# Performance work log

Hardware: AMD Instinct MI355X
Metric: run time of the kernel (lower is better)

Reference implementation:

```python
import jax, jax.numpy as jnp
import numpy as np

PAD = (2, 2)  # from kernel=[1,3,3,1], sampling_factor_padding=2, kernel_size=3


def _make_kernel(k1d):
    k = np.asarray(k1d, dtype=np.float32)
    k2d = k[None, :] * k[:, None]
    return jnp.asarray(k2d / k2d.sum())


def setup_inputs() -> dict:
    key = jax.random.key(0)
    x = jax.random.normal(key, (8, 256, 256, 256), dtype=jnp.float32)
    kernel = _make_kernel([1, 3, 3, 1])  # [4,4] normalized FIR kernel (buffer)
    return {"x": x, "kernel": kernel}


def reference(x, kernel):
    # upfirdn2d with up=1, down=1, pad=(2,2): pad then depthwise TRUE convolution
    # (StyleGAN2 flips the kernel before F.conv2d, i.e. real convolution).
    B, C, H, W = x.shape
    kh, kw = kernel.shape
    w = jnp.flip(kernel, (0, 1)).astype(x.dtype)[None, None]  # [1,1,kh,kw]
    w = jnp.broadcast_to(w, (C, 1, kh, kw))  # depthwise: same kernel per channel
    out = jax.lax.conv_general_dilated(
        x, w,
        window_strides=(1, 1),
        padding=(PAD, PAD),
        dimension_numbers=("NCHW", "OIHW", "NCHW"),
        feature_group_count=C,
    )  # [B, C, H+1, W+1] since H + 4 - 4 + 1 = H + 1
    return out
```

## Files before the change

kernel.cpp:

```cpp
#include <hip/hip_runtime.h>


#define IW 256
#define IH 256
#define OW 257
#define OH 257

typedef float f4u __attribute__((vector_size(16), aligned(4)));

__device__ __forceinline__ float sbc(float v) {
    return __uint_as_float(__builtin_amdgcn_readfirstlane(__float_as_uint(v)));
}

__global__ __launch_bounds__(256) void blur_fir_kernel(
    const float* __restrict__ x,
    const float* __restrict__ k2d,
    float* __restrict__ out)
{
    const int tid   = threadIdx.x;
    const int cg    = tid & 63;
    const int strip = tid >> 6;
    const int plane = blockIdx.x;

    const float w0 = sbc(k2d[0]);
    const float w1 = sbc(k2d[1]);
    const float w2 = sbc(k2d[2]);
    const float w3 = sbc(k2d[3]);
    const float inv = 1.0f / w0;
    const float v1 = sbc(k2d[4]  * inv);
    const float v2 = sbc(k2d[8]  * inv);
    const float v3 = sbc(k2d[12] * inv);

    const int   c0 = cg << 2;
    const float mL = (cg > 0)  ? 1.0f : 0.0f;
    const float mR = (cg < 63) ? 1.0f : 0.0f;
    const int   lm = (cg > 0)  ? cg - 1 : 0;
    const int   lp = (cg < 63) ? cg + 1 : 63;

    const float* xp = x + ((size_t)plane << 16);
    const int r0 = strip << 6;

    auto loadraw = [&](int r) -> float4 {
        int rr = min(max(r, 0), IH - 1);
        return *(const float4*)(xp + (rr << 8) + c0);
    };
    auto hcomb = [&](float4 Bv, int r, float4& h, float& h4) {
        float rm = (r >= 0 && r < IH) ? 1.0f : 0.0f;
        float lx = __shfl(Bv.z, lm, 64) * mL;
        float ly = __shfl(Bv.w, lm, 64) * mL;
        float rv = __shfl(Bv.x, lp, 64) * mR;
        h.x = w0 * Bv.y + w1 * Bv.x + w2 * ly   + w3 * lx;
        h.y = w0 * Bv.z + w1 * Bv.y + w2 * Bv.x + w3 * ly;
        h.z = w0 * Bv.w + w1 * Bv.z + w2 * Bv.y + w3 * Bv.x;
        h.w = w0 * rv   + w1 * Bv.w + w2 * Bv.z + w3 * Bv.y;
        h4  = w2 * Bv.w + w3 * Bv.z;
        h.x *= rm; h.y *= rm; h.z *= rm; h.w *= rm; h4 *= rm;
    };
    auto vcomb = [&](float4 a, float4 b, float4 c, float4 d) -> float4 {
        float4 r;
        r.x = a.x + v1 * b.x + v2 * c.x + v3 * d.x;
        r.y = a.y + v1 * b.y + v2 * c.y + v3 * d.y;
        r.z = a.z + v1 * b.z + v2 * c.z + v3 * d.z;
        r.w = a.w + v1 * b.w + v2 * c.w + v3 * d.w;
        return r;
    };

    float4 C0, C1, C2; float sc0, sc1, sc2;
    { float4 B = loadraw(r0 - 2); hcomb(B, r0 - 2, C0, sc0); }
    { float4 B = loadraw(r0 - 1); hcomb(B, r0 - 1, C1, sc1); }
    { float4 B = loadraw(r0    ); hcomb(B, r0    , C2, sc2); }

    float4 G0 = loadraw(r0 + 1);
    float4 G1 = loadraw(r0 + 2);
    float4 G2 = loadraw(r0 + 3);
    float4 G3 = loadraw(r0 + 4);

    float* op = out + (size_t)plane * (OW * OH) + (size_t)r0 * OW + c0;
    const bool last = (cg == 63);

    #pragma unroll 2
    for (int g = 0; g < 16; ++g) {
        const int rb = r0 + (g << 2);
        float4 N0 = loadraw(rb + 5);
        float4 N1 = loadraw(rb + 6);
        float4 N2 = loadraw(rb + 7);
        float4 N3 = loadraw(rb + 8);

        float4 F0, F1, F2, F3; float sf0, sf1, sf2, sf3;
        hcomb(G0, rb + 1, F0, sf0);
        hcomb(G1, rb + 2, F1, sf1);
        hcomb(G2, rb + 3, F2, sf2);
        hcomb(G3, rb + 4, F3, sf3);

        float4 R0 = vcomb(F0, C2, C1, C0);
        float4 R1 = vcomb(F1, F0, C2, C1);
        float4 R2 = vcomb(F2, F1, F0, C2);
        float4 R3 = vcomb(F3, F2, F1, F0);
        *(f4u*)(op         ) = (f4u){R0.x, R0.y, R0.z, R0.w};
        *(f4u*)(op +     OW) = (f4u){R1.x, R1.y, R1.z, R1.w};
        *(f4u*)(op + 2 * OW) = (f4u){R2.x, R2.y, R2.z, R2.w};
        *(f4u*)(op + 3 * OW) = (f4u){R3.x, R3.y, R3.z, R3.w};
        if (last) {
            op[4]          = sf0 + v1 * sc2 + v2 * sc1 + v3 * sc0;
            op[OW + 4]     = sf1 + v1 * sf0 + v2 * sc2 + v3 * sc1;
            op[2 * OW + 4] = sf2 + v1 * sf1 + v2 * sf0 + v3 * sc2;
            op[3 * OW + 4] = sf3 + v1 * sf2 + v2 * sf1 + v3 * sf0;
        }
        op += 4 * OW;

        C0 = F1;  C1 = F2;  C2 = F3;
        sc0 = sf1; sc1 = sf2; sc2 = sf3;
        G0 = N0; G1 = N1; G2 = N2; G3 = N3;
    }

    if (strip == 3) {
        float4 R;
        R.x = v1 * C2.x + v2 * C1.x + v3 * C0.x;
        R.y = v1 * C2.y + v2 * C1.y + v3 * C0.y;
        R.z = v1 * C2.z + v2 * C1.z + v3 * C0.z;
        R.w = v1 * C2.w + v2 * C1.w + v3 * C0.w;
        *(f4u*)op = (f4u){R.x, R.y, R.z, R.w};
        if (last) op[4] = v1 * sc2 + v2 * sc1 + v3 * sc0;
    }
}

extern "C" void kernel_launch(void* const* d_in, const int* in_sizes, int n_in,
                              void* d_out, int out_size, void* d_ws, size_t ws_size,
                              hipStream_t stream) {
    const float* x   = (const float*)d_in[0];
    const float* k2d = (const float*)d_in[1];
    float* out = (float*)d_out;

    int nplanes = in_sizes[0] >> 16;
    blur_fir_kernel<<<nplanes, 256, 0, stream>>>(x, k2d, out);
}
```

Baseline: 247.4 us.

## Process two planes per block with deeper 8-row register pipeline

Each block now handles two consecutive planes in sequence and half as many blocks are launched. The inner row loop advances 8 rows per iteration with 8 prefetched rows in flight instead of 4, and launch bounds request 4 waves per SIMD. The goal is more outstanding loads per wave to hide memory latency and less per-block setup cost. In exchange it uses more registers, risks a tighter occupancy limit, and halves the block count, which reduces parallelism across CUs (1024 blocks).

```diff
diff --git a/kernel.cpp b/kernel.cpp
--- a/kernel.cpp
+++ b/kernel.cpp
@@ -12,7 +12,7 @@
     return __uint_as_float(__builtin_amdgcn_readfirstlane(__float_as_uint(v)));
 }
 
-__global__ __launch_bounds__(256) void blur_fir_kernel(
+__global__ __launch_bounds__(256, 4) void blur_fir_kernel(
     const float* __restrict__ x,
     const float* __restrict__ k2d,
     float* __restrict__ out)
@@ -20,7 +20,6 @@
     const int tid   = threadIdx.x;
     const int cg    = tid & 63;
     const int strip = tid >> 6;
-    const int plane = blockIdx.x;
 
     const float w0 = sbc(k2d[0]);
     const float w1 = sbc(k2d[1]);
@@ -36,91 +35,111 @@
     const float mR = (cg < 63) ? 1.0f : 0.0f;
     const int   lm = (cg > 0)  ? cg - 1 : 0;
     const int   lp = (cg < 63) ? cg + 1 : 63;
-
-    const float* xp = x + ((size_t)plane << 16);
-    const int r0 = strip << 6;
-
-    auto loadraw = [&](int r) -> float4 {
-        int rr = min(max(r, 0), IH - 1);
-        return *(const float4*)(xp + (rr << 8) + c0);
-    };
-    auto hcomb = [&](float4 Bv, int r, float4& h, float& h4) {
-        float rm = (r >= 0 && r < IH) ? 1.0f : 0.0f;
-        float lx = __shfl(Bv.z, lm, 64) * mL;
-        float ly = __shfl(Bv.w, lm, 64) * mL;
-        float rv = __shfl(Bv.x, lp, 64) * mR;
-        h.x = w0 * Bv.y + w1 * Bv.x + w2 * ly   + w3 * lx;
-        h.y = w0 * Bv.z + w1 * Bv.y + w2 * Bv.x + w3 * ly;
-        h.z = w0 * Bv.w + w1 * Bv.z + w2 * Bv.y + w3 * Bv.x;
-        h.w = w0 * rv   + w1 * Bv.w + w2 * Bv.z + w3 * Bv.y;
-        h4  = w2 * Bv.w + w3 * Bv.z;
-        h.x *= rm; h.y *= rm; h.z *= rm; h.w *= rm; h4 *= rm;
-    };
-    auto vcomb = [&](float4 a, float4 b, float4 c, float4 d) -> float4 {
-        float4 r;
-        r.x = a.x + v1 * b.x + v2 * c.x + v3 * d.x;
-        r.y = a.y + v1 * b.y + v2 * c.y + v3 * d.y;
-        r.z = a.z + v1 * b.z + v2 * c.z + v3 * d.z;
-        r.w = a.w + v1 * b.w + v2 * c.w + v3 * d.w;
-        return r;
-    };
-
-    float4 C0, C1, C2; float sc0, sc1, sc2;
-    { float4 B = loadraw(r0 - 2); hcomb(B, r0 - 2, C0, sc0); }
-    { float4 B = loadraw(r0 - 1); hcomb(B, r0 - 1, C1, sc1); }
-    { float4 B = loadraw(r0    ); hcomb(B, r0    , C2, sc2); }
-
-    float4 G0 = loadraw(r0 + 1);
-    float4 G1 = loadraw(r0 + 2);
-    float4 G2 = loadraw(r0 + 3);
-    float4 G3 = loadraw(r0 + 4);
-
-    float* op = out + (size_t)plane * (OW * OH) + (size_t)r0 * OW + c0;
+    const int   r0 = strip << 6;
     const bool last = (cg == 63);
 
-    #pragma unroll 2
-    for (int g = 0; g < 16; ++g) {
-        const int rb = r0 + (g << 2);
-        float4 N0 = loadraw(rb + 5);
-        float4 N1 = loadraw(rb + 6);
-        float4 N2 = loadraw(rb + 7);
-        float4 N3 = loadraw(rb + 8);
+    for (int pp = 0; pp < 2; ++pp) {
+        const int plane = (blockIdx.x << 1) + pp;
+        const float* xp = x + ((size_t)plane << 16);
 
-        float4 F0, F1, F2, F3; float sf0, sf1, sf2, sf3;
-        hcomb(G0, rb + 1, F0, sf0);
-        hcomb(G1, rb + 2, F1, sf1);
-        hcomb(G2, rb + 3, F2, sf2);
-        hcomb(G3, rb + 4, F3, sf3);
+        auto loadraw = [&](int r) -> float4 {
+            int rr = min(max(r, 0), IH - 1);
+            return *(const float4*)(xp + (rr << 8) + c0);
+        };
+        auto hcomb = [&](float4 Bv, int r, float4& h, float& h4) {
+            float rm = (r >= 0 && r < IH) ? 1.0f : 0.0f;
+            float lx = __shfl(Bv.z, lm, 64) * mL;
+            float ly = __shfl(Bv.w, lm, 64) * mL;
+            float rv = __shfl(Bv.x, lp, 64) * mR;
+            h.x = w0 * Bv.y + w1 * Bv.x + w2 * ly   + w3 * lx;
+            h.y = w0 * Bv.z + w1 * Bv.y + w2 * Bv.x + w3 * ly;
+            h.z = w0 * Bv.w + w1 * Bv.z + w2 * Bv.y + w3 * Bv.x;
+            h.w = w0 * rv   + w1 * Bv.w + w2 * Bv.z + w3 * Bv.y;
+            h4  = w2 * Bv.w + w3 * Bv.z;
+            h.x *= rm; h.y *= rm; h.z *= rm; h.w *= rm; h4 *= rm;
+        };
+        auto vcomb = [&](float4 a, float4 b, float4 c, float4 d) -> float4 {
+            float4 r;
+            r.x = a.x + v1 * b.x + v2 * c.x + v3 * d.x;
+            r.y = a.y + v1 * b.y + v2 * c.y + v3 * d.y;
+            r.z = a.z + v1 * b.z + v2 * c.z + v3 * d.z;
+            r.w = a.w + v1 * b.w + v2 * c.w + v3 * d.w;
+            return r;
+        };
 
-        float4 R0 = vcomb(F0, C2, C1, C0);
-        float4 R1 = vcomb(F1, F0, C2, C1);
-        float4 R2 = vcomb(F2, F1, F0, C2);
-        float4 R3 = vcomb(F3, F2, F1, F0);
-        *(f4u*)(op         ) = (f4u){R0.x, R0.y, R0.z, R0.w};
-        *(f4u*)(op +     OW) = (f4u){R1.x, R1.y, R1.z, R1.w};
-        *(f4u*)(op + 2 * OW) = (f4u){R2.x, R2.y, R2.z, R2.w};
-        *(f4u*)(op + 3 * OW) = (f4u){R3.x, R3.y, R3.z, R3.w};
-        if (last) {
-            op[4]          = sf0 + v1 * sc2 + v2 * sc1 + v3 * sc0;
-            op[OW + 4]     = sf1 + v1 * sf0 + v2 * sc2 + v3 * sc1;
-            op[2 * OW + 4] = sf2 + v1 * sf1 + v2 * sf0 + v3 * sc2;
-            op[3 * OW + 4] = sf3 + v1 * sf2 + v2 * sf1 + v3 * sf0;
+        float4 C0, C1, C2; float sc0, sc1, sc2;
+        { float4 B = loadraw(r0 - 2); hcomb(B, r0 - 2, C0, sc0); }
+        { float4 B = loadraw(r0 - 1); hcomb(B, r0 - 1, C1, sc1); }
+        { float4 B = loadraw(r0    ); hcomb(B, r0    , C2, sc2); }
+        float4 G0 = loadraw(r0 + 1), G1 = loadraw(r0 + 2);
+        float4 G2 = loadraw(r0 + 3), G3 = loadraw(r0 + 4);
+        float4 G4 = loadraw(r0 + 5), G5 = loadraw(r0 + 6);
+        float4 G6 = loadraw(r0 + 7), G7 = loadraw(r0 + 8);
+
+        float* op = out + (size_t)plane * (OW * OH) + (size_t)r0 * OW + c0;
+
+        #pragma unroll 2
+        for (int g = 0; g < 8; ++g) {
+            const int rb = r0 + (g << 3);
+            float4 N0 = loadraw(rb + 9),  N1 = loadraw(rb + 10);
+            float4 N2 = loadraw(rb + 11), N3 = loadraw(rb + 12);
+            float4 N4 = loadraw(rb + 13), N5 = loadraw(rb + 14);
+            float4 N6 = loadraw(rb + 15), N7 = loadraw(rb + 16);
+
+            float4 F0, F1, F2, F3, F4, F5, F6, F7;
+            float  sf0, sf1, sf2, sf3, sf4, sf5, sf6, sf7;
+            hcomb(G0, rb + 1, F0, sf0);
+            hcomb(G1, rb + 2, F1, sf1);
+            hcomb(G2, rb + 3, F2, sf2);
+            hcomb(G3, rb + 4, F3, sf3);
+            hcomb(G4, rb + 5, F4, sf4);
+            hcomb(G5, rb + 6, F5, sf5);
+            hcomb(G6, rb + 7, F6, sf6);
+            hcomb(G7, rb + 8, F7, sf7);
+
+            float4 R0 = vcomb(F0, C2, C1, C0);
+            float4 R1 = vcomb(F1, F0, C2, C1);
+            float4 R2 = vcomb(F2, F1, F0, C2);
+            float4 R3 = vcomb(F3, F2, F1, F0);
+            float4 R4 = vcomb(F4, F3, F2, F1);
+            float4 R5 = vcomb(F5, F4, F3, F2);
+            float4 R6 = vcomb(F6, F5, F4, F3);
+            float4 R7 = vcomb(F7, F6, F5, F4);
+            *(f4u*)(op         ) = (f4u){R0.x, R0.y, R0.z, R0.w};
+            *(f4u*)(op +     OW) = (f4u){R1.x, R1.y, R1.z, R1.w};
+            *(f4u*)(op + 2 * OW) = (f4u){R2.x, R2.y, R2.z, R2.w};
+            *(f4u*)(op + 3 * OW) = (f4u){R3.x, R3.y, R3.z, R3.w};
+            *(f4u*)(op + 4 * OW) = (f4u){R4.x, R4.y, R4.z, R4.w};
+            *(f4u*)(op + 5 * OW) = (f4u){R5.x, R5.y, R5.z, R5.w};
+            *(f4u*)(op + 6 * OW) = (f4u){R6.x, R6.y, R6.z, R6.w};
+            *(f4u*)(op + 7 * OW) = (f4u){R7.x, R7.y, R7.z, R7.w};
+            if (last) {
+                op[4]          = sf0 + v1 * sc2 + v2 * sc1 + v3 * sc0;
+                op[OW + 4]     = sf1 + v1 * sf0 + v2 * sc2 + v3 * sc1;
+                op[2 * OW + 4] = sf2 + v1 * sf1 + v2 * sf0 + v3 * sc2;
+                op[3 * OW + 4] = sf3 + v1 * sf2 + v2 * sf1 + v3 * sf0;
+                op[4 * OW + 4] = sf4 + v1 * sf3 + v2 * sf2 + v3 * sf1;
+                op[5 * OW + 4] = sf5 + v1 * sf4 + v2 * sf3 + v3 * sf2;
+                op[6 * OW + 4] = sf6 + v1 * sf5 + v2 * sf4 + v3 * sf3;
+                op[7 * OW + 4] = sf7 + v1 * sf6 + v2 * sf5 + v3 * sf4;
+            }
+            op += 8 * OW;
+
+            C0 = F5;  C1 = F6;  C2 = F7;
+            sc0 = sf5; sc1 = sf6; sc2 = sf7;
+            G0 = N0; G1 = N1; G2 = N2; G3 = N3;
+            G4 = N4; G5 = N5; G6 = N6; G7 = N7;
         }
-        op += 4 * OW;
 
-        C0 = F1;  C1 = F2;  C2 = F3;
-        sc0 = sf1; sc1 = sf2; sc2 = sf3;
-        G0 = N0; G1 = N1; G2 = N2; G3 = N3;
-    }
-
-    if (strip == 3) {
-        float4 R;
-        R.x = v1 * C2.x + v2 * C1.x + v3 * C0.x;
-        R.y = v1 * C2.y + v2 * C1.y + v3 * C0.y;
-        R.z = v1 * C2.z + v2 * C1.z + v3 * C0.z;
-        R.w = v1 * C2.w + v2 * C1.w + v3 * C0.w;
-        *(f4u*)op = (f4u){R.x, R.y, R.z, R.w};
-        if (last) op[4] = v1 * sc2 + v2 * sc1 + v3 * sc0;
+        if (strip == 3) {
+            float4 R;
+            R.x = v1 * C2.x + v2 * C1.x + v3 * C0.x;
+            R.y = v1 * C2.y + v2 * C1.y + v3 * C0.y;
+            R.z = v1 * C2.z + v2 * C1.z + v3 * C0.z;
+            R.w = v1 * C2.w + v2 * C1.w + v3 * C0.w;
+            *(f4u*)op = (f4u){R.x, R.y, R.z, R.w};
+            if (last) op[4] = v1 * sc2 + v2 * sc1 + v3 * sc0;
+        }
     }
 }
 
@@ -132,5 +151,6 @@
     float* out = (float*)d_out;
 
     int nplanes = in_sizes[0] >> 16;
-    blur_fir_kernel<<<nplanes, 256, 0, stream>>>(x, k2d, out);
+    int nblocks = nplanes >> 1;
+    blur_fir_kernel<<<nblocks, 256, 0, stream>>>(x, k2d, out);
 }
```

Result: slower. 272.2 us (+10.0%).

## Split work into 4-row wave tasks with grid-stride persistent scheduling

Applied to the files above, without the earlier changes.

Replaces the one-block-per-plane layout, where each wave streams 64 rows, with a grid of 2048 blocks whose waves take independent tasks of 4 output rows each in a grid-stride loop. Each task reloads its 7 input rows, so no horizontal results are carried between tasks. This aims to even out load balance and memory-level parallelism across CUs. In exchange, about 7/4 times as many input rows are read and horizontally filtered, which relies on L2 to absorb the overlapping reads.

```diff
diff --git a/kernel.cpp b/kernel.cpp
--- a/kernel.cpp
+++ b/kernel.cpp
@@ -5,6 +5,7 @@
 #define IH 256
 #define OW 257
 #define OH 257
+#define NG 65
 
 typedef float f4u __attribute__((vector_size(16), aligned(4)));
 
@@ -15,12 +16,11 @@
 __global__ __launch_bounds__(256) void blur_fir_kernel(
     const float* __restrict__ x,
     const float* __restrict__ k2d,
-    float* __restrict__ out)
+    float* __restrict__ out,
+    int ntasks, int nwaves)
 {
-    const int tid   = threadIdx.x;
-    const int cg    = tid & 63;
-    const int strip = tid >> 6;
-    const int plane = blockIdx.x;
+    const int lane = threadIdx.x & 63;
+    const int gw   = (blockIdx.x << 2) + (threadIdx.x >> 6);
 
     const float w0 = sbc(k2d[0]);
     const float w1 = sbc(k2d[1]);
@@ -31,96 +31,87 @@
     const float v2 = sbc(k2d[8]  * inv);
     const float v3 = sbc(k2d[12] * inv);
 
-    const int   c0 = cg << 2;
-    const float mL = (cg > 0)  ? 1.0f : 0.0f;
-    const float mR = (cg < 63) ? 1.0f : 0.0f;
-    const int   lm = (cg > 0)  ? cg - 1 : 0;
-    const int   lp = (cg < 63) ? cg + 1 : 63;
+    const int   c0 = lane << 2;
+    const float mL = (lane > 0)  ? 1.0f : 0.0f;
+    const float mR = (lane < 63) ? 1.0f : 0.0f;
+    const int   lm = (lane > 0)  ? lane - 1 : 0;
+    const int   lp = (lane < 63) ? lane + 1 : 63;
+    const bool last = (lane == 63);
 
-    const float* xp = x + ((size_t)plane << 16);
-    const int r0 = strip << 6;
+    for (int t = gw; t < ntasks; t += nwaves) {
+        const int plane = t / NG;
+        const int rg    = t - plane * NG;
+        const float* xp = x + ((size_t)plane << 16);
+        float* op = out + (size_t)plane * (OW * OH) + (size_t)(rg << 2) * OW + c0;
 
-    auto loadraw = [&](int r) -> float4 {
-        int rr = min(max(r, 0), IH - 1);
-        return *(const float4*)(xp + (rr << 8) + c0);
-    };
-    auto hcomb = [&](float4 Bv, int r, float4& h, float& h4) {
-        float rm = (r >= 0 && r < IH) ? 1.0f : 0.0f;
-        float lx = __shfl(Bv.z, lm, 64) * mL;
-        float ly = __shfl(Bv.w, lm, 64) * mL;
-        float rv = __shfl(Bv.x, lp, 64) * mR;
-        h.x = w0 * Bv.y + w1 * Bv.x + w2 * ly   + w3 * lx;
-        h.y = w0 * Bv.z + w1 * Bv.y + w2 * Bv.x + w3 * ly;
-        h.z = w0 * Bv.w + w1 * Bv.z + w2 * Bv.y + w3 * Bv.x;
-        h.w = w0 * rv   + w1 * Bv.w + w2 * Bv.z + w3 * Bv.y;
-        h4  = w2 * Bv.w + w3 * Bv.z;
-        h.x *= rm; h.y *= rm; h.z *= rm; h.w *= rm; h4 *= rm;
-    };
-    auto vcomb = [&](float4 a, float4 b, float4 c, float4 d) -> float4 {
-        float4 r;
-        r.x = a.x + v1 * b.x + v2 * c.x + v3 * d.x;
-        r.y = a.y + v1 * b.y + v2 * c.y + v3 * d.y;
-        r.z = a.z + v1 * b.z + v2 * c.z + v3 * d.z;
-        r.w = a.w + v1 * b.w + v2 * c.w + v3 * d.w;
-        return r;
-    };
+        auto loadraw = [&](int r) -> float4 {
+            int rr = min(max(r, 0), IH - 1);
+            return *(const float4*)(xp + (rr << 8) + c0);
+        };
+        auto hcomb = [&](float4 Bv, int r, float4& h, float& h4) {
+            float rm = (r >= 0 && r < IH) ? 1.0f : 0.0f;
+            float lx = __shfl(Bv.z, lm, 64) * mL;
+            float ly = __shfl(Bv.w, lm, 64) * mL;
+            float rv = __shfl(Bv.x, lp, 64) * mR;
+            h.x = w0 * Bv.y + w1 * Bv.x + w2 * ly   + w3 * lx;
+            h.y = w0 * Bv.z + w1 * Bv.y + w2 * Bv.x + w3 * ly;
+            h.z = w0 * Bv.w + w1 * Bv.z + w2 * Bv.y + w3 * Bv.x;
+            h.w = w0 * rv   + w1 * Bv.w + w2 * Bv.z + w3 * Bv.y;
+            h4  = w2 * Bv.w + w3 * Bv.z;
+            h.x *= rm; h.y *= rm; h.z *= rm; h.w *= rm; h4 *= rm;
+        };
+        auto vcomb = [&](float4 a, float4 b, float4 c, float4 d) -> float4 {
+            float4 r;
+            r.x = a.x + v1 * b.x + v2 * c.x + v3 * d.x;
+            r.y = a.y + v1 * b.y + v2 * c.y + v3 * d.y;
+            r.z = a.z + v1 * b.z + v2 * c.z + v3 * d.z;
+            r.w = a.w + v1 * b.w + v2 * c.w + v3 * d.w;
+            return r;
+        };
 
-    float4 C0, C1, C2; float sc0, sc1, sc2;
-    { float4 B = loadraw(r0 - 2); hcomb(B, r0 - 2, C0, sc0); }
-    { float4 B = loadraw(r0 - 1); hcomb(B, r0 - 1, C1, sc1); }
-    { float4 B = loadraw(r0    ); hcomb(B, r0    , C2, sc2); }
+        if (rg < 64) {
+            const int rb = rg << 2;
+            float4 G0 = loadraw(rb - 2), G1 = loadraw(rb - 1), G2 = loadraw(rb);
+            float4 G3 = loadraw(rb + 1), G4 = loadraw(rb + 2), G5 = loadraw(rb + 3);
+            float4 G6 = loadraw(rb + 4);
 
-    float4 G0 = loadraw(r0 + 1);
-    float4 G1 = loadraw(r0 + 2);
-    float4 G2 = loadraw(r0 + 3);
-    float4 G3 = loadraw(r0 + 4);
+            float4 F0, F1, F2, F3, F4, F5, F6;
+            float  s0, s1, s2, s3, s4, s5, s6;
+            hcomb(G0, rb - 2, F0, s0);
+            hcomb(G1, rb - 1, F1, s1);
+            hcomb(G2, rb    , F2, s2);
+            hcomb(G3, rb + 1, F3, s3);
+            hcomb(G4, rb + 2, F4, s4);
+            hcomb(G5, rb + 3, F5, s5);
+            hcomb(G6, rb + 4, F6, s6);
 
-    float* op = out + (size_t)plane * (OW * OH) + (size_t)r0 * OW + c0;
-    const bool last = (cg == 63);
-
-    #pragma unroll 2
-    for (int g = 0; g < 16; ++g) {
-        const int rb = r0 + (g << 2);
-        float4 N0 = loadraw(rb + 5);
-        float4 N1 = loadraw(rb + 6);
-        float4 N2 = loadraw(rb + 7);
-        float4 N3 = loadraw(rb + 8);
-
-        float4 F0, F1, F2, F3; float sf0, sf1, sf2, sf3;
-        hcomb(G0, rb + 1, F0, sf0);
-        hcomb(G1, rb + 2, F1, sf1);
-        hcomb(G2, rb + 3, F2, sf2);
-        hcomb(G3, rb + 4, F3, sf3);
-
-        float4 R0 = vcomb(F0, C2, C1, C0);
-        float4 R1 = vcomb(F1, F0, C2, C1);
-        float4 R2 = vcomb(F2, F1, F0, C2);
-        float4 R3 = vcomb(F3, F2, F1, F0);
-        *(f4u*)(op         ) = (f4u){R0.x, R0.y, R0.z, R0.w};
-        *(f4u*)(op +     OW) = (f4u){R1.x, R1.y, R1.z, R1.w};
-        *(f4u*)(op + 2 * OW) = (f4u){R2.x, R2.y, R2.z, R2.w};
-        *(f4u*)(op + 3 * OW) = (f4u){R3.x, R3.y, R3.z, R3.w};
-        if (last) {
-            op[4]          = sf0 + v1 * sc2 + v2 * sc1 + v3 * sc0;
-            op[OW + 4]     = sf1 + v1 * sf0 + v2 * sc2 + v3 * sc1;
-            op[2 * OW + 4] = sf2 + v1 * sf1 + v2 * sf0 + v3 * sc2;
-            op[3 * OW + 4] = sf3 + v1 * sf2 + v2 * sf1 + v3 * sf0;
+            float4 R0 = vcomb(F3, F2, F1, F0);
+            float4 R1 = vcomb(F4, F3, F2, F1);
+            float4 R2 = vcomb(F5, F4, F3, F2);
+            float4 R3 = vcomb(F6, F5, F4, F3);
+            *(f4u*)(op         ) = (f4u){R0.x, R0.y, R0.z, R0.w};
+            *(f4u*)(op +     OW) = (f4u){R1.x, R1.y, R1.z, R1.w};
+            *(f4u*)(op + 2 * OW) = (f4u){R2.x, R2.y, R2.z, R2.w};
+            *(f4u*)(op + 3 * OW) = (f4u){R3.x, R3.y, R3.z, R3.w};
+            if (last) {
+                op[4]          = s3 + v1 * s2 + v2 * s1 + v3 * s0;
+                op[OW + 4]     = s4 + v1 * s3 + v2 * s2 + v3 * s1;
+                op[2 * OW + 4] = s5 + v1 * s4 + v2 * s3 + v3 * s2;
+                op[3 * OW + 4] = s6 + v1 * s5 + v2 * s4 + v3 * s3;
+            }
+        } else {
+            float4 GA = loadraw(254), GB = loadraw(255);
+            float4 FA, FB; float sA, sB;
+            hcomb(GA, 254, FA, sA);
+            hcomb(GB, 255, FB, sB);
+            float4 R;
+            R.x = v2 * FB.x + v3 * FA.x;
+            R.y = v2 * FB.y + v3 * FA.y;
+            R.z = v2 * FB.z + v3 * FA.z;
+            R.w = v2 * FB.w + v3 * FA.w;
+            *(f4u*)op = (f4u){R.x, R.y, R.z, R.w};
+            if (last) op[4] = v2 * sB + v3 * sA;
         }
-        op += 4 * OW;
-
-        C0 = F1;  C1 = F2;  C2 = F3;
-        sc0 = sf1; sc1 = sf2; sc2 = sf3;
-        G0 = N0; G1 = N1; G2 = N2; G3 = N3;
-    }
-
-    if (strip == 3) {
-        float4 R;
-        R.x = v1 * C2.x + v2 * C1.x + v3 * C0.x;
-        R.y = v1 * C2.y + v2 * C1.y + v3 * C0.y;
-        R.z = v1 * C2.z + v2 * C1.z + v3 * C0.z;
-        R.w = v1 * C2.w + v2 * C1.w + v3 * C0.w;
-        *(f4u*)op = (f4u){R.x, R.y, R.z, R.w};
-        if (last) op[4] = v1 * sc2 + v2 * sc1 + v3 * sc0;
     }
 }
 
@@ -132,5 +123,9 @@
     float* out = (float*)d_out;
 
     int nplanes = in_sizes[0] >> 16;
-    blur_fir_kernel<<<nplanes, 256, 0, stream>>>(x, k2d, out);
+    int ntasks  = nplanes * NG;
+    int nblocks = 2048;
+    int nwaves  = nblocks * 4;
+
+    blur_fir_kernel<<<nblocks, 256, 0, stream>>>(x, k2d, out, ntasks, nwaves);
 }
```

Result: faster. 234.6 us (-5.2%).

## Stage input rows into a per-wave LDS ring via async global-to-LDS loads

Applied to the files above, without the earlier changes.

Input rows are no longer prefetched into registers. They are copied asynchronously into a per-wave 8-slot LDS ring buffer with global_load_lds, and the left and right neighbour values come from LDS reads instead of cross-lane shuffles. A vmcnt wait is placed so each iteration's rows are resident while the next four rows are in flight. This aims to cut register pressure and shuffle cost and to keep more loads outstanding. In exchange it uses 32 KB of LDS per block, which may reduce occupancy, relies on hand-placed waitcnt ordering, and drops the loop unroll.

```diff
diff --git a/kernel.cpp b/kernel.cpp
--- a/kernel.cpp
+++ b/kernel.cpp
@@ -5,6 +5,7 @@
 #define IH 256
 #define OW 257
 #define OH 257
+#define NSLOT 8
 
 typedef float f4u __attribute__((vector_size(16), aligned(4)));
 
@@ -12,15 +13,26 @@
     return __uint_as_float(__builtin_amdgcn_readfirstlane(__float_as_uint(v)));
 }
 
+__device__ __forceinline__ void gld16(const float* g, float* l) {
+    __builtin_amdgcn_global_load_lds(
+        (const __attribute__((address_space(1))) void*)g,
+        (__attribute__((address_space(3))) void*)l, 16, 0, 0);
+}
+
+#define WAIT_VM(n)   asm volatile("s_waitcnt vmcnt(" #n ")" ::: "memory")
+#define WAIT_LGKM0() asm volatile("s_waitcnt lgkmcnt(0)" ::: "memory")
+
 __global__ __launch_bounds__(256) void blur_fir_kernel(
     const float* __restrict__ x,
     const float* __restrict__ k2d,
     float* __restrict__ out)
 {
-    const int tid   = threadIdx.x;
-    const int cg    = tid & 63;
-    const int strip = tid >> 6;
+    __shared__ float L[4][NSLOT * 256];
+
+    const int lane  = threadIdx.x & 63;
+    const int wv    = threadIdx.x >> 6;
     const int plane = blockIdx.x;
+    const int r0    = wv << 6;
 
     const float w0 = sbc(k2d[0]);
     const float w1 = sbc(k2d[1]);
@@ -31,24 +43,27 @@
     const float v2 = sbc(k2d[8]  * inv);
     const float v3 = sbc(k2d[12] * inv);
 
-    const int   c0 = cg << 2;
-    const float mL = (cg > 0)  ? 1.0f : 0.0f;
-    const float mR = (cg < 63) ? 1.0f : 0.0f;
-    const int   lm = (cg > 0)  ? cg - 1 : 0;
-    const int   lp = (cg < 63) ? cg + 1 : 63;
+    const int   c0   = lane << 2;
+    const float mL   = (lane > 0)  ? 1.0f : 0.0f;
+    const float mR   = (lane < 63) ? 1.0f : 0.0f;
+    const int   offL = (lane > 0)  ? c0 - 2 : 0;
+    const int   offR = (lane < 63) ? c0 + 4 : 0;
+    const bool  last = (lane == 63);
 
     const float* xp = x + ((size_t)plane << 16);
-    const int r0 = strip << 6;
+    float* Lw = L[wv];
 
-    auto loadraw = [&](int r) -> float4 {
+    auto stage = [&](int r) {
         int rr = min(max(r, 0), IH - 1);
-        return *(const float4*)(xp + (rr << 8) + c0);
+        gld16(xp + (rr << 8) + c0, Lw + ((r & (NSLOT - 1)) << 8));
     };
-    auto hcomb = [&](float4 Bv, int r, float4& h, float& h4) {
+    auto hcombL = [&](int r, float4& h, float& h4) {
+        const float* rowp = Lw + ((r & (NSLOT - 1)) << 8);
         float rm = (r >= 0 && r < IH) ? 1.0f : 0.0f;
-        float lx = __shfl(Bv.z, lm, 64) * mL;
-        float ly = __shfl(Bv.w, lm, 64) * mL;
-        float rv = __shfl(Bv.x, lp, 64) * mR;
+        float2 Lv = *(const float2*)(rowp + offL);
+        float4 Bv = *(const float4*)(rowp + c0);
+        float  Rv = rowp[offR];
+        float lx = Lv.x * mL, ly = Lv.y * mL, rv = Rv * mR;
         h.x = w0 * Bv.y + w1 * Bv.x + w2 * ly   + w3 * lx;
         h.y = w0 * Bv.z + w1 * Bv.y + w2 * Bv.x + w3 * ly;
         h.z = w0 * Bv.w + w1 * Bv.z + w2 * Bv.y + w3 * Bv.x;
@@ -65,32 +80,32 @@
         return r;
     };
 
+    stage(r0 - 2); stage(r0 - 1); stage(r0);
+    stage(r0 + 1); stage(r0 + 2); stage(r0 + 3); stage(r0 + 4);
+    WAIT_VM(0);
+    __builtin_amdgcn_sched_barrier(0);
+
     float4 C0, C1, C2; float sc0, sc1, sc2;
-    { float4 B = loadraw(r0 - 2); hcomb(B, r0 - 2, C0, sc0); }
-    { float4 B = loadraw(r0 - 1); hcomb(B, r0 - 1, C1, sc1); }
-    { float4 B = loadraw(r0    ); hcomb(B, r0    , C2, sc2); }
-
-    float4 G0 = loadraw(r0 + 1);
-    float4 G1 = loadraw(r0 + 2);
-    float4 G2 = loadraw(r0 + 3);
-    float4 G3 = loadraw(r0 + 4);
+    hcombL(r0 - 2, C0, sc0);
+    hcombL(r0 - 1, C1, sc1);
+    hcombL(r0,     C2, sc2);
+    WAIT_LGKM0();
+    __builtin_amdgcn_sched_barrier(0);
 
     float* op = out + (size_t)plane * (OW * OH) + (size_t)r0 * OW + c0;
-    const bool last = (cg == 63);
 
-    #pragma unroll 2
-    for (int g = 0; g < 16; ++g) {
-        const int rb = r0 + (g << 2);
-        float4 N0 = loadraw(rb + 5);
-        float4 N1 = loadraw(rb + 6);
-        float4 N2 = loadraw(rb + 7);
-        float4 N3 = loadraw(rb + 8);
+    #pragma unroll 1
+    for (int i = 0; i < 16; ++i) {
+        const int a = r0 + (i << 2);
+        stage(a + 5); stage(a + 6); stage(a + 7); stage(a + 8);
+        WAIT_VM(8);
+        __builtin_amdgcn_sched_barrier(0);
 
         float4 F0, F1, F2, F3; float sf0, sf1, sf2, sf3;
-        hcomb(G0, rb + 1, F0, sf0);
-        hcomb(G1, rb + 2, F1, sf1);
-        hcomb(G2, rb + 3, F2, sf2);
-        hcomb(G3, rb + 4, F3, sf3);
+        hcombL(a + 1, F0, sf0);
+        hcombL(a + 2, F1, sf1);
+        hcombL(a + 3, F2, sf2);
+        hcombL(a + 4, F3, sf3);
 
         float4 R0 = vcomb(F0, C2, C1, C0);
         float4 R1 = vcomb(F1, F0, C2, C1);
@@ -110,17 +125,16 @@
 
         C0 = F1;  C1 = F2;  C2 = F3;
         sc0 = sf1; sc1 = sf2; sc2 = sf3;
-        G0 = N0; G1 = N1; G2 = N2; G3 = N3;
     }
 
-    if (strip == 3) {
+    if (wv == 3) {
         float4 R;
-        R.x = v1 * C2.x + v2 * C1.x + v3 * C0.x;
-        R.y = v1 * C2.y + v2 * C1.y + v3 * C0.y;
-        R.z = v1 * C2.z + v2 * C1.z + v3 * C0.z;
-        R.w = v1 * C2.w + v2 * C1.w + v3 * C0.w;
+        R.x = v2 * C1.x + v3 * C0.x;
+        R.y = v2 * C1.y + v3 * C0.y;
+        R.z = v2 * C1.z + v3 * C0.z;
+        R.w = v2 * C1.w + v3 * C0.w;
         *(f4u*)op = (f4u){R.x, R.y, R.z, R.w};
-        if (last) op[4] = v1 * sc2 + v2 * sc1 + v3 * sc0;
+        if (last) op[4] = v2 * sc1 + v3 * sc0;
     }
 }
 
```

Result: no change. 251.5 us (+1.6%).
